# Kernel tuning notes

Measured on AMD Instinct MI355X. Metric: run time of the kernel, lower is better.

The kernel has to match this reference:

```python
import jax, jax.numpy as jnp
import numpy as np

N, E = 100000, 1200000
IN, HC = 3, 64
FC1, FC2, FC3, OUT = 64, 32, 16, 3
BN_EPS = 1e-5


def _lin(key, fan_in, fan_out):
    # kaiming-uniform-ish init, zero bias (as in parameter_init)
    bound = np.sqrt(6.0 / fan_in)
    w = jax.random.uniform(key, (fan_in, fan_out), minval=-bound, maxval=bound, dtype=jnp.float32)
    return w, jnp.zeros((fan_out,), jnp.float32)


def setup_inputs() -> dict:
    key = jax.random.key(0)
    ks = jax.random.split(key, 16)
    x = jax.random.normal(ks[0], (N, IN), dtype=jnp.float32)
    edge_index = jax.random.randint(ks[1], (2, E), 0, N, dtype=jnp.int64)
    d = {"x": x, "edge_index": edge_index}
    # EdgeConv MLPs: Linear(2*c_in, hc) -> ReLU -> Linear(hc, hc)
    d["w1a"], d["b1a"] = _lin(ks[2], 2 * IN, HC)
    d["w1b"], d["b1b"] = _lin(ks[3], HC, HC)
    d["w2a"], d["b2a"] = _lin(ks[4], 2 * HC, HC)
    d["w2b"], d["b2b"] = _lin(ks[5], HC, HC)
    d["w3a"], d["b3a"] = _lin(ks[6], 2 * HC, HC)
    d["w3b"], d["b3b"] = _lin(ks[7], HC, HC)
    # BatchNorm (eval mode) params per layer: gamma, beta, running_mean, running_var
    for i in (1, 2, 3):
        d[f"bn{i}_g"] = jnp.ones((HC,), jnp.float32)
        d[f"bn{i}_b"] = jnp.zeros((HC,), jnp.float32)
        d[f"bn{i}_m"] = jnp.zeros((HC,), jnp.float32)
        d[f"bn{i}_v"] = jnp.ones((HC,), jnp.float32)
    # dense head
    d["lw1"], d["lb1"] = _lin(ks[8], HC, FC1)
    d["lw2"], d["lb2"] = _lin(ks[9], FC1, FC2)
    d["lw3"], d["lb3"] = _lin(ks[10], FC2, FC3)
    d["lw4"], d["lb4"] = _lin(ks[11], FC3, OUT)
    return d


def _edge_conv(x, src, dst, wa, ba, wb, bb):
    # PyG EdgeConv: message = mlp(cat[x_i, x_j - x_i]), max-aggregated at target i
    x_i = x[dst]                              # [E, C]
    x_j = x[src]                              # [E, C]
    h = jnp.concatenate([x_i, x_j - x_i], axis=-1)   # [E, 2C]
    h = jax.nn.relu(h @ wa + ba) @ wb + bb           # [E, HC]
    agg = jax.ops.segment_max(h, dst, num_segments=x.shape[0])
    return jnp.where(jnp.isfinite(agg), agg, 0.0)    # isolated nodes -> 0


def _bn(x, g, b, m, v):
    return (x - m) * jax.lax.rsqrt(v + BN_EPS) * g + b


def reference(x, edge_index,
              w1a, b1a, w1b, b1b, w2a, b2a, w2b, b2b, w3a, b3a, w3b, b3b,
              bn1_g, bn1_b, bn1_m, bn1_v, bn2_g, bn2_b, bn2_m, bn2_v,
              bn3_g, bn3_b, bn3_m, bn3_v,
              lw1, lb1, lw2, lb2, lw3, lb3, lw4, lb4):
    src, dst = edge_index[0], edge_index[1]
    h = _edge_conv(x, src, dst, w1a, b1a, w1b, b1b)
    h = jax.nn.relu(_bn(h, bn1_g, bn1_b, bn1_m, bn1_v))
    h = _edge_conv(h, src, dst, w2a, b2a, w2b, b2b)
    h = jax.nn.relu(_bn(h, bn2_g, bn2_b, bn2_m, bn2_v))
    h = _edge_conv(h, src, dst, w3a, b3a, w3b, b3b)
    h = jax.nn.relu(_bn(h, bn3_g, bn3_b, bn3_m, bn3_v))
    h = jax.nn.relu(h @ lw1 + lb1)
    h = jax.nn.relu(h @ lw2 + lb2)
    h = jax.nn.relu(h @ lw3 + lb3)
    return h @ lw4 + lb4
```

## Files before the change

### kernel.cpp

```cpp
#include <hip/hip_runtime.h>

#define CAP 64
#define BN_EPS 1e-5f

typedef _Float16 f16;
typedef _Float16 half8 __attribute__((ext_vector_type(8)));
typedef float f32x4 __attribute__((ext_vector_type(4)));

__global__ __launch_bounds__(256) void build_buckets(
    const int* __restrict__ ei, int E,
    int* __restrict__ deg, int* __restrict__ bucket)
{
    int e = blockIdx.x * blockDim.x + threadIdx.x;
    if (e >= E) return;
    int src = ei[e];
    int dst = ei[E + e];
    int slot = atomicAdd(&deg[dst], 1);
    if (slot < CAP) bucket[dst * CAP + slot] = src;
}

__global__ __launch_bounds__(256) void uv_kernel(
    const float* __restrict__ feat, int ldf, int K, int N,
    const float* __restrict__ wa, const float* __restrict__ ba,
    f16* __restrict__ U, f16* __restrict__ V)
{
    __shared__ float Wlds[2][64][64];
    __shared__ float blds[64];
    int tid = threadIdx.x;
    for (int idx = tid; idx < 2 * K * 64; idx += blockDim.x) {
        int half = idx / (K * 64);
        int rem = idx - half * (K * 64);
        int k = rem >> 6, o = rem & 63;
        float wB = wa[(K + k) * 64 + o];
        Wlds[half][k][o] = (half == 0) ? (wa[k * 64 + o] - wB) : wB;
    }
    if (tid < 64) blds[tid] = ba[tid];
    __syncthreads();

    int t = blockIdx.x * blockDim.x + tid;
    if (t >= 2 * N) return;
    int node = t >> 1, half = t & 1;

    float acc[64];
    #pragma unroll
    for (int o = 0; o < 64; ++o) acc[o] = (half == 0) ? blds[o] : 0.f;

    const float* f = feat + (long)node * ldf;
    for (int k = 0; k < K; ++k) {
        float c = f[k];
        #pragma unroll
        for (int o = 0; o < 64; ++o) acc[o] = fmaf(c, Wlds[half][k][o], acc[o]);
    }
    f16* dstp = (half == 0 ? U : V) + (long)node * 64;
    #pragma unroll
    for (int o = 0; o < 64; o += 8) {
        half8 h;
        #pragma unroll
        for (int j = 0; j < 8; ++j) h[j] = (f16)acc[o + j];
        *(half8*)(dstp + o) = h;
    }
}

__global__ __launch_bounds__(256, 4) void node_kernel(
    const f16* __restrict__ U, const f16* __restrict__ V,
    const int* __restrict__ deg, const int* __restrict__ bucket,
    const float* __restrict__ wb, const float* __restrict__ bb,
    const float* __restrict__ bng, const float* __restrict__ bnb,
    const float* __restrict__ bnm, const float* __restrict__ bnv,
    int N, float* __restrict__ Fout)
{
    const int lane = threadIdx.x & 63;
    const int r16 = lane >> 4, c16 = lane & 15;
    const int wid = (blockIdx.x * blockDim.x + threadIdx.x) >> 6;
    const int nwaves = (gridDim.x * blockDim.x) >> 6;

    __shared__ half8 WB[8][64];
    for (int idx = threadIdx.x; idx < 8 * 64; idx += blockDim.x) {
        int f = idx >> 6, l = idx & 63;
        int lr = l >> 4, lc = l & 15;
        int s = f & 1, ct = f >> 1;
        half8 h;
        #pragma unroll
        for (int j = 0; j < 8; ++j) {
            int k = 32 * s + 8 * lr + j;
            h[j] = (f16)wb[k * 64 + 16 * ct + lc];
        }
        WB[f][l] = h;
    }
    __syncthreads();

    const float bbv = bb[lane];
    const float g = bng[lane], be = bnb[lane];
    const float rs = rsqrtf(bnv[lane] + BN_EPS), mm = bnm[lane];

    int chunk = (N + nwaves - 1) / nwaves;
    int n0 = wid * chunk;
    int n1 = n0 + chunk; if (n1 > N) n1 = N;
    if (n0 >= n1) return;

    int dval = 0;
    if (lane < n1 - n0) dval = deg[n0 + lane];
    dval = dval > CAP ? CAP : dval;

    auto nclamp = [&](int n) { return n < n1 ? n : n1 - 1; };

    int bkt0 = bucket[(long)n0 * CAP + c16];
    int bkt1 = bucket[(long)nclamp(n0 + 1) * CAP + c16];
    int bkt2 = bucket[(long)nclamp(n0 + 2) * CAP + c16];

    unsigned s0 = (unsigned)bkt0 < (unsigned)N ? (unsigned)bkt0 : 0u;
    unsigned s1 = (unsigned)bkt1 < (unsigned)N ? (unsigned)bkt1 : 0u;
    const half8* vp0 = (const half8*)(V + (long)s0 * 64);
    const half8* vp1 = (const half8*)(V + (long)s1 * 64);
    half8 v0A = vp0[r16], v0B = vp0[4 + r16];
    half8 v1A = vp1[r16], v1B = vp1[4 + r16];
    const half8* up0 = (const half8*)(U + (long)n0 * 64);
    half8 u0A = up0[r16], u0B = up0[4 + r16];

    for (int node = n0; node < n1; ++node) {
        unsigned s2 = (unsigned)bkt2 < (unsigned)N ? (unsigned)bkt2 : 0u;
        const half8* vp2 = (const half8*)(V + (long)s2 * 64);
        half8 v2A = vp2[r16], v2B = vp2[4 + r16];
        int bkt3 = bucket[(long)nclamp(node + 3) * CAP + c16];
        const half8* up1 = (const half8*)(U + (long)nclamp(node + 1) * 64);
        half8 u1A = up1[r16], u1B = up1[4 + r16];

        int d = __shfl(dval, node - n0);

        float m0 = -INFINITY, m1 = -INFINITY, m2 = -INFINITY, m3 = -INFINITY;
        int ntile = (d + 15) >> 4;

        if (ntile > 0) {
            half8 a0 = v0A + u0A;
            half8 a1 = v0B + u0B;
            #pragma unroll
            for (int j = 0; j < 8; ++j) {
                a0[j] = a0[j] > (f16)0 ? a0[j] : (f16)0;
                a1[j] = a1[j] > (f16)0 ? a1[j] : (f16)0;
            }
            const f32x4 z = {0.f, 0.f, 0.f, 0.f};
            #pragma unroll
            for (int ct = 0; ct < 4; ++ct) {
                f32x4 acc = __builtin_amdgcn_mfma_f32_16x16x32_f16(a0, WB[ct * 2 + 0][lane], z, 0, 0, 0);
                acc = __builtin_amdgcn_mfma_f32_16x16x32_f16(a1, WB[ct * 2 + 1][lane], acc, 0, 0, 0);
                float mx = -INFINITY;
                #pragma unroll
                for (int r = 0; r < 4; ++r) {
                    int row = r16 * 4 + r;
                    float val = (row < d) ? acc[r] : -INFINITY;
                    mx = fmaxf(mx, val);
                }
                mx = fmaxf(mx, __shfl_xor(mx, 16));
                mx = fmaxf(mx, __shfl_xor(mx, 32));
                if (ct == 0) m0 = fmaxf(m0, mx);
                else if (ct == 1) m1 = fmaxf(m1, mx);
                else if (ct == 2) m2 = fmaxf(m2, mx);
                else m3 = fmaxf(m3, mx);
            }
        }
        for (int t = 1; t < ntile; ++t) {
            int bkt = bucket[(long)node * CAP + t * 16 + c16];
            unsigned su = (unsigned)bkt < (unsigned)N ? (unsigned)bkt : 0u;
            const half8* vrt = (const half8*)(V + (long)su * 64);
            half8 a0 = vrt[r16] + u0A;
            half8 a1 = vrt[4 + r16] + u0B;
            #pragma unroll
            for (int j = 0; j < 8; ++j) {
                a0[j] = a0[j] > (f16)0 ? a0[j] : (f16)0;
                a1[j] = a1[j] > (f16)0 ? a1[j] : (f16)0;
            }
            const f32x4 z = {0.f, 0.f, 0.f, 0.f};
            #pragma unroll
            for (int ct = 0; ct < 4; ++ct) {
                f32x4 acc = __builtin_amdgcn_mfma_f32_16x16x32_f16(a0, WB[ct * 2 + 0][lane], z, 0, 0, 0);
                acc = __builtin_amdgcn_mfma_f32_16x16x32_f16(a1, WB[ct * 2 + 1][lane], acc, 0, 0, 0);
                float mx = -INFINITY;
                #pragma unroll
                for (int r = 0; r < 4; ++r) {
                    int row = t * 16 + r16 * 4 + r;
                    float val = (row < d) ? acc[r] : -INFINITY;
                    mx = fmaxf(mx, val);
                }
                mx = fmaxf(mx, __shfl_xor(mx, 16));
                mx = fmaxf(mx, __shfl_xor(mx, 32));
                if (ct == 0) m0 = fmaxf(m0, mx);
                else if (ct == 1) m1 = fmaxf(m1, mx);
                else if (ct == 2) m2 = fmaxf(m2, mx);
                else m3 = fmaxf(m3, mx);
            }
        }

        float sel = (r16 == 0) ? m0 : (r16 == 1) ? m1 : (r16 == 2) ? m2 : m3;
        float aggv = (d > 0) ? sel + bbv : 0.f;
        float bn = (aggv - mm) * rs * g + be;
        Fout[(long)node * 64 + lane] = fmaxf(bn, 0.f);

        v0A = v1A; v0B = v1B; v1A = v2A; v1B = v2B;
        u0A = u1A; u0B = u1B;
        bkt2 = bkt3;
    }
}

__global__ __launch_bounds__(256) void head_kernel(
    const float* __restrict__ F,
    const float* __restrict__ lw1, const float* __restrict__ lb1,
    const float* __restrict__ lw2, const float* __restrict__ lb2,
    const float* __restrict__ lw3, const float* __restrict__ lb3,
    const float* __restrict__ lw4, const float* __restrict__ lb4,
    int N, float* __restrict__ out)
{
    __shared__ float W1[64][64];
    __shared__ float W2[64][32];
    __shared__ float W3[32][16];
    __shared__ float W4[16][3];
    __shared__ float B1[64], B2[32], B3[16], B4[3];
    int tid = threadIdx.x;
    for (int i = tid; i < 64 * 64; i += blockDim.x) W1[i >> 6][i & 63] = lw1[i];
    for (int i = tid; i < 64 * 32; i += blockDim.x) W2[i >> 5][i & 31] = lw2[i];
    for (int i = tid; i < 32 * 16; i += blockDim.x) W3[i >> 4][i & 15] = lw3[i];
    for (int i = tid; i < 16 * 3;  i += blockDim.x) W4[i / 3][i % 3]  = lw4[i];
    if (tid < 64) B1[tid] = lb1[tid];
    if (tid < 32) B2[tid] = lb2[tid];
    if (tid < 16) B3[tid] = lb3[tid];
    if (tid < 3)  B4[tid] = lb4[tid];
    __syncthreads();

    int n = blockIdx.x * blockDim.x + tid;
    if (n >= N) return;
    const float* f = F + (long)n * 64;

    float h1[64];
    #pragma unroll
    for (int o = 0; o < 64; ++o) h1[o] = B1[o];
    for (int k = 0; k < 64; ++k) {
        float c = f[k];
        #pragma unroll
        for (int o = 0; o < 64; ++o) h1[o] = fmaf(c, W1[k][o], h1[o]);
    }
    float h2[32];
    #pragma unroll
    for (int o = 0; o < 32; ++o) h2[o] = B2[o];
    #pragma unroll
    for (int k = 0; k < 64; ++k) {
        float c = fmaxf(h1[k], 0.f);
        #pragma unroll
        for (int o = 0; o < 32; ++o) h2[o] = fmaf(c, W2[k][o], h2[o]);
    }
    float h3[16];
    #pragma unroll
    for (int o = 0; o < 16; ++o) h3[o] = B3[o];
    #pragma unroll
    for (int k = 0; k < 32; ++k) {
        float c = fmaxf(h2[k], 0.f);
        #pragma unroll
        for (int o = 0; o < 16; ++o) h3[o] = fmaf(c, W3[k][o], h3[o]);
    }
    float o0 = B4[0], o1 = B4[1], o2 = B4[2];
    #pragma unroll
    for (int k = 0; k < 16; ++k) {
        float c = fmaxf(h3[k], 0.f);
        o0 = fmaf(c, W4[k][0], o0);
        o1 = fmaf(c, W4[k][1], o1);
        o2 = fmaf(c, W4[k][2], o2);
    }
    out[(long)n * 3 + 0] = o0;
    out[(long)n * 3 + 1] = o1;
    out[(long)n * 3 + 2] = o2;
}

extern "C" void kernel_launch(void* const* d_in, const int* in_sizes, int n_in,
                              void* d_out, int out_size, void* d_ws, size_t ws_size,
                              hipStream_t stream)
{
    const float* x   = (const float*)d_in[0];
    const int*   ei  = (const int*)d_in[1];
    int N = in_sizes[0] / 3;
    int E = in_sizes[1] / 2;

    const float* w1a = (const float*)d_in[2];  const float* b1a = (const float*)d_in[3];
    const float* w1b = (const float*)d_in[4];  const float* b1b = (const float*)d_in[5];
    const float* w2a = (const float*)d_in[6];  const float* b2a = (const float*)d_in[7];
    const float* w2b = (const float*)d_in[8];  const float* b2b = (const float*)d_in[9];
    const float* w3a = (const float*)d_in[10]; const float* b3a = (const float*)d_in[11];
    const float* w3b = (const float*)d_in[12]; const float* b3b = (const float*)d_in[13];
    const float* bn1g = (const float*)d_in[14]; const float* bn1b = (const float*)d_in[15];
    const float* bn1m = (const float*)d_in[16]; const float* bn1v = (const float*)d_in[17];
    const float* bn2g = (const float*)d_in[18]; const float* bn2b = (const float*)d_in[19];
    const float* bn2m = (const float*)d_in[20]; const float* bn2v = (const float*)d_in[21];
    const float* bn3g = (const float*)d_in[22]; const float* bn3b = (const float*)d_in[23];
    const float* bn3m = (const float*)d_in[24]; const float* bn3v = (const float*)d_in[25];
    const float* lw1 = (const float*)d_in[26]; const float* lb1 = (const float*)d_in[27];
    const float* lw2 = (const float*)d_in[28]; const float* lb2 = (const float*)d_in[29];
    const float* lw3 = (const float*)d_in[30]; const float* lb3 = (const float*)d_in[31];
    const float* lw4 = (const float*)d_in[32]; const float* lb4 = (const float*)d_in[33];
    float* out = (float*)d_out;

    char* ws = (char*)d_ws;
    size_t off = 0;
    auto alloc = [&](size_t bytes) { void* p = ws + off; off += (bytes + 255) & ~(size_t)255; return p; };
    int*   deg    = (int*)  alloc((size_t)N * sizeof(int));
    int*   bucket = (int*)  alloc((size_t)N * CAP * sizeof(int));
    f16*   U      = (f16*)  alloc((size_t)N * 64 * sizeof(f16));
    f16*   V      = (f16*)  alloc((size_t)N * 64 * sizeof(f16));
    float* F      = (float*)alloc((size_t)N * 64 * sizeof(float));
    (void)ws_size; (void)n_in; (void)out_size;

    hipMemsetAsync(deg, 0, (size_t)N * sizeof(int), stream);
    build_buckets<<<(E + 255) / 256, 256, 0, stream>>>(ei, E, deg, bucket);

    int uv_grid   = (2 * N + 255) / 256;
    int node_blocks = 2048;
    int nd_grid   = (N + 255) / 256;

    uv_kernel<<<uv_grid, 256, 0, stream>>>(x, 3, 3, N, w1a, b1a, U, V);
    node_kernel<<<node_blocks, 256, 0, stream>>>(U, V, deg, bucket, w1b, b1b,
                                                 bn1g, bn1b, bn1m, bn1v, N, F);
    uv_kernel<<<uv_grid, 256, 0, stream>>>(F, 64, 64, N, w2a, b2a, U, V);
    node_kernel<<<node_blocks, 256, 0, stream>>>(U, V, deg, bucket, w2b, b2b,
                                                 bn2g, bn2b, bn2m, bn2v, N, F);
    uv_kernel<<<uv_grid, 256, 0, stream>>>(F, 64, 64, N, w3a, b3a, U, V);
    node_kernel<<<node_blocks, 256, 0, stream>>>(U, V, deg, bucket, w3b, b3b,
                                                 bn3g, bn3b, bn3m, bn3v, N, F);
    head_kernel<<<nd_grid, 256, 0, stream>>>(F, lw1, lb1, lw2, lb2, lw3, lb3,
                                             lw4, lb4, N, out);
}
```

Before: 558.2 us.

## Split UV projection across 16 threads per node and store node features in fp16

The U/V projection kernel now assigns 16 threads per node, each computing 8 output channels, instead of 2 threads each computing all 64. That cuts per-thread register pressure and raises parallelism, and the K dimension becomes a template parameter so loops fully unroll. Intermediate node features F are now written and read as fp16 instead of fp32, halving that traffic through the node, UV and head kernels. The trade-off is lower precision in the inter-layer activations, and each of the 16 threads per node re-reads the full feature row.

```diff
diff --git a/kernel.cpp b/kernel.cpp
--- a/kernel.cpp
+++ b/kernel.cpp
@@ -19,15 +19,16 @@
     if (slot < CAP) bucket[dst * CAP + slot] = src;
 }
 
-__global__ __launch_bounds__(256) void uv_kernel(
-    const float* __restrict__ feat, int ldf, int K, int N,
+template<typename T, int K>
+__global__ __launch_bounds__(256) void uv2_kernel(
+    const T* __restrict__ feat, int N,
     const float* __restrict__ wa, const float* __restrict__ ba,
     f16* __restrict__ U, f16* __restrict__ V)
 {
-    __shared__ float Wlds[2][64][64];
+    __shared__ float Wlds[2][K][64];
     __shared__ float blds[64];
     int tid = threadIdx.x;
-    for (int idx = tid; idx < 2 * K * 64; idx += blockDim.x) {
+    for (int idx = tid; idx < 2 * K * 64; idx += 256) {
         int half = idx / (K * 64);
         int rem = idx - half * (K * 64);
         int k = rem >> 6, o = rem & 63;
@@ -37,28 +38,51 @@
     if (tid < 64) blds[tid] = ba[tid];
     __syncthreads();
 
-    int t = blockIdx.x * blockDim.x + tid;
-    if (t >= 2 * N) return;
-    int node = t >> 1, half = t & 1;
-
-    float acc[64];
-    #pragma unroll
-    for (int o = 0; o < 64; ++o) acc[o] = (half == 0) ? blds[o] : 0.f;
-
-    const float* f = feat + (long)node * ldf;
-    for (int k = 0; k < K; ++k) {
-        float c = f[k];
-        #pragma unroll
-        for (int o = 0; o < 64; ++o) acc[o] = fmaf(c, Wlds[half][k][o], acc[o]);
-    }
-    f16* dstp = (half == 0 ? U : V) + (long)node * 64;
-    #pragma unroll
-    for (int o = 0; o < 64; o += 8) {
-        half8 h;
-        #pragma unroll
-        for (int j = 0; j < 8; ++j) h[j] = (f16)acc[o + j];
-        *(half8*)(dstp + o) = h;
-    }
+    long t = (long)blockIdx.x * 256 + tid;
+    if (t >= (long)N * 16) return;
+    int node = (int)(t >> 4);
+    int sub = (int)(t & 15);
+    int half = sub >> 3;
+    int og = (sub & 7) * 8;
+
+    float acc[8];
+    #pragma unroll
+    for (int j = 0; j < 8; ++j) acc[j] = (half == 0) ? blds[og + j] : 0.f;
+
+    if constexpr (K == 3) {
+        const T* f = feat + (long)node * K;
+        #pragma unroll
+        for (int k = 0; k < 3; ++k) {
+            float c = (float)f[k];
+            float4 w0 = *(const float4*)&Wlds[half][k][og];
+            float4 w1 = *(const float4*)&Wlds[half][k][og + 4];
+            acc[0] = fmaf(c, w0.x, acc[0]); acc[1] = fmaf(c, w0.y, acc[1]);
+            acc[2] = fmaf(c, w0.z, acc[2]); acc[3] = fmaf(c, w0.w, acc[3]);
+            acc[4] = fmaf(c, w1.x, acc[4]); acc[5] = fmaf(c, w1.y, acc[5]);
+            acc[6] = fmaf(c, w1.z, acc[6]); acc[7] = fmaf(c, w1.w, acc[7]);
+        }
+    } else {
+        const half8* fp = (const half8*)(feat + (long)node * K);
+        half8 fr[K / 8];
+        #pragma unroll
+        for (int q = 0; q < K / 8; ++q) fr[q] = fp[q];
+        #pragma unroll
+        for (int k = 0; k < K; ++k) {
+            float c = (float)fr[k >> 3][k & 7];
+            float4 w0 = *(const float4*)&Wlds[half][k][og];
+            float4 w1 = *(const float4*)&Wlds[half][k][og + 4];
+            acc[0] = fmaf(c, w0.x, acc[0]); acc[1] = fmaf(c, w0.y, acc[1]);
+            acc[2] = fmaf(c, w0.z, acc[2]); acc[3] = fmaf(c, w0.w, acc[3]);
+            acc[4] = fmaf(c, w1.x, acc[4]); acc[5] = fmaf(c, w1.y, acc[5]);
+            acc[6] = fmaf(c, w1.z, acc[6]); acc[7] = fmaf(c, w1.w, acc[7]);
+        }
+    }
+
+    half8 h;
+    #pragma unroll
+    for (int j = 0; j < 8; ++j) h[j] = (f16)acc[j];
+    f16* dstp = (half == 0 ? U : V) + (long)node * 64 + og;
+    *(half8*)dstp = h;
 }
 
 __global__ __launch_bounds__(256, 4) void node_kernel(
@@ -67,7 +91,7 @@
     const float* __restrict__ wb, const float* __restrict__ bb,
     const float* __restrict__ bng, const float* __restrict__ bnb,
     const float* __restrict__ bnm, const float* __restrict__ bnv,
-    int N, float* __restrict__ Fout)
+    int N, f16* __restrict__ Fout)
 {
     const int lane = threadIdx.x & 63;
     const int r16 = lane >> 4, c16 = lane & 15;
@@ -193,7 +217,7 @@
         float sel = (r16 == 0) ? m0 : (r16 == 1) ? m1 : (r16 == 2) ? m2 : m3;
         float aggv = (d > 0) ? sel + bbv : 0.f;
         float bn = (aggv - mm) * rs * g + be;
-        Fout[(long)node * 64 + lane] = fmaxf(bn, 0.f);
+        Fout[(long)node * 64 + lane] = (f16)fmaxf(bn, 0.f);
 
         v0A = v1A; v0B = v1B; v1A = v2A; v1B = v2B;
         u0A = u1A; u0B = u1B;
@@ -202,7 +226,7 @@
 }
 
 __global__ __launch_bounds__(256) void head_kernel(
-    const float* __restrict__ F,
+    const f16* __restrict__ F,
     const float* __restrict__ lw1, const float* __restrict__ lb1,
     const float* __restrict__ lw2, const float* __restrict__ lb2,
     const float* __restrict__ lw3, const float* __restrict__ lb3,
@@ -227,13 +251,13 @@
 
     int n = blockIdx.x * blockDim.x + tid;
     if (n >= N) return;
-    const float* f = F + (long)n * 64;
+    const f16* f = F + (long)n * 64;
 
     float h1[64];
     #pragma unroll
     for (int o = 0; o < 64; ++o) h1[o] = B1[o];
     for (int k = 0; k < 64; ++k) {
-        float c = f[k];
+        float c = (float)f[k];
         #pragma unroll
         for (int o = 0; o < 64; ++o) h1[o] = fmaf(c, W1[k][o], h1[o]);
     }
@@ -302,23 +326,24 @@
     int*   bucket = (int*)  alloc((size_t)N * CAP * sizeof(int));
     f16*   U      = (f16*)  alloc((size_t)N * 64 * sizeof(f16));
     f16*   V      = (f16*)  alloc((size_t)N * 64 * sizeof(f16));
-    float* F      = (float*)alloc((size_t)N * 64 * sizeof(float));
+    f16*   F      = (f16*)  alloc((size_t)N * 64 * sizeof(f16));
     (void)ws_size; (void)n_in; (void)out_size;
 
     hipMemsetAsync(deg, 0, (size_t)N * sizeof(int), stream);
     build_buckets<<<(E + 255) / 256, 256, 0, stream>>>(ei, E, deg, bucket);
 
-    int uv_grid   = (2 * N + 255) / 256;
+    long uv_threads = (long)N * 16;
+    int uv_grid   = (int)((uv_threads + 255) / 256);
     int node_blocks = 2048;
     int nd_grid   = (N + 255) / 256;
 
-    uv_kernel<<<uv_grid, 256, 0, stream>>>(x, 3, 3, N, w1a, b1a, U, V);
+    uv2_kernel<float, 3><<<uv_grid, 256, 0, stream>>>(x, N, w1a, b1a, U, V);
     node_kernel<<<node_blocks, 256, 0, stream>>>(U, V, deg, bucket, w1b, b1b,
                                                  bn1g, bn1b, bn1m, bn1v, N, F);
-    uv_kernel<<<uv_grid, 256, 0, stream>>>(F, 64, 64, N, w2a, b2a, U, V);
+    uv2_kernel<f16, 64><<<uv_grid, 256, 0, stream>>>(F, N, w2a, b2a, U, V);
     node_kernel<<<node_blocks, 256, 0, stream>>>(U, V, deg, bucket, w2b, b2b,
                                                  bn2g, bn2b, bn2m, bn2v, N, F);
-    uv_kernel<<<uv_grid, 256, 0, stream>>>(F, 64, 64, N, w3a, b3a, U, V);
+    uv2_kernel<f16, 64><<<uv_grid, 256, 0, stream>>>(F, N, w3a, b3a, U, V);
     node_kernel<<<node_blocks, 256, 0, stream>>>(U, V, deg, bucket, w3b, b3b,
                                                  bn3g, bn3b, bn3m, bn3v, N, F);
     head_kernel<<<nd_grid, 256, 0, stream>>>(F, lw1, lb1, lw2, lb2, lw3, lb3,
```

Measured after the change: 550.1 us. About the same (-1.5%).
